# Performance work log

Measured on AMD Instinct MI355X. Metric: run time of the kernel, lower is better.

Reference implementation:

```python
import jax, jax.numpy as jnp
import numpy as np

EPS = 1e-10


def _entropy(feat):
    # feat: [B,S,D] -> [B,S]
    fa = jnp.abs(feat)
    fn = fa / (fa.sum(axis=-1, keepdims=True) + EPS)
    return -jnp.sum(fn * jnp.log(fn + EPS), axis=-1)


def setup_inputs() -> dict:
    key = jax.random.key(0)
    ks = jax.random.split(key, 16)
    B, S, H, C = 16, 1024, 512, 7
    inp = {
        'text': jax.random.normal(ks[0], (B, S, H), dtype=jnp.float32),
        'audio': jax.random.normal(ks[1], (B, S, H), dtype=jnp.float32),
        'visual': jax.random.normal(ks[2], (B, S, H), dtype=jnp.float32),
        'speaker_graph': jax.random.uniform(ks[3], (B, S, S), dtype=jnp.float32),
        'temporal_graph': jax.random.uniform(ks[4], (B, S, S), dtype=jnp.float32),
        'qmask': jax.random.randint(ks[5], (B, S), 0, 9, dtype=jnp.int64),
        # entropy gate linear: in = 3H+1, out = H  (stored as [in,out])
        'gate_W': jax.random.normal(ks[6], (3 * H + 1, H), dtype=jnp.float32) * 0.02,
        'gate_b': jnp.zeros((H,), dtype=jnp.float32),
        # spectral conv layers
        'W0': jax.random.normal(ks[7], (3 * H, H), dtype=jnp.float32) * 0.02,
        'b0': jnp.zeros((H,), dtype=jnp.float32),
        'W1': jax.random.normal(ks[8], (H, H), dtype=jnp.float32) * 0.02,
        'b1': jnp.zeros((H,), dtype=jnp.float32),
        'W2': jax.random.normal(ks[9], (H, H), dtype=jnp.float32) * 0.02,
        'b2': jnp.zeros((H,), dtype=jnp.float32),
        # classifier
        'Wc': jax.random.normal(ks[10], (H, C), dtype=jnp.float32) * 0.02,
        'bc': jnp.zeros((C,), dtype=jnp.float32),
    }
    return inp


def reference(text, audio, visual, speaker_graph, temporal_graph, qmask,
              gate_W, gate_b, W0, b0, W1, b1, W2, b2, Wc, bc):
    feats = {'text': text, 'audio': audio, 'visual': visual}
    names = list(feats.keys())

    # per-node entropy on speaker graph path (entropy_t computed but unused, as in source)
    ent_s = {m: _entropy(f) for m, f in feats.items()}

    # entropy-weighted gating per modality
    fused = {}
    for m in names:
        feat = feats[m]
        ref = jnp.mean(jnp.stack([feats[o] for o in names if o != m], axis=-1), axis=-1)
        gi = jnp.concatenate([feat, feat, ref, ent_s[m][..., None]], axis=-1)  # [B,S,3H+1]
        gate = jax.nn.sigmoid(gi @ gate_W + gate_b)
        fused[m] = gate * feat

    # spectral GNN: symmetric-normalized fused adjacency with self loops
    B, S = text.shape[0], text.shape[1]
    fused_adj = 0.5 * speaker_graph + 0.5 * temporal_graph
    fused_adj = fused_adj + jnp.eye(S, dtype=fused_adj.dtype)[None]
    D = fused_adj.sum(axis=-1)                                   # [B,S]
    dsi = jax.lax.rsqrt(D + EPS)                                  # (D+eps)^-0.5
    norm_adj = dsi[:, :, None] * fused_adj * dsi[:, None, :]      # [B,S,S]

    h = jnp.concatenate([fused['text'], fused['audio'], fused['visual']], axis=-1)  # [B,S,3H]
    for W, b in ((W0, b0), (W1, b1), (W2, b2)):
        h = jax.nn.relu(jnp.einsum('bij,bjd->bid', norm_adj, h @ W) + b)

    return h @ Wc + bc
```

## Files before the change

### kernel.cpp

```cpp
#include <hip/hip_runtime.h>
#include <hip/hip_bf16.h>
#include <hip/hip_fp16.h>

typedef _Float16 f16;
typedef __attribute__((ext_vector_type(8))) _Float16 f16x8;
typedef __attribute__((ext_vector_type(4))) _Float16 f16x4;
typedef __attribute__((ext_vector_type(4))) float f32x4;

#define BQ 16
#define SQ 1024
#define HQ 512
#define MQ (BQ*SQ)
#define PLANE ((size_t)MQ*512)

#define OFF_WG1T 0ul
#define OFF_WG2T 524288ul
#define OFF_W0T  1048576ul
#define OFF_W1T  2621440ul
#define OFF_W2T  3145728ul
#define OFF_WENT 3670016ul
#define OFF_ENTS 3672064ul
#define OFF_DSI  3868672ul
#define OFF_XF16 3934208ul
#define OFF_ANORM OFF_XF16
#define OFF_HN   (OFF_XF16 + 33554432ul)
#define OFF_T    71043072ul
#define OFF_YT   OFF_T
#define OFF_HCAT 104597504ul

__global__ __launch_bounds__(256) void k_prep(
    const float* __restrict__ gW, const float* __restrict__ W0,
    const float* __restrict__ W1, const float* __restrict__ W2,
    f16* __restrict__ Wg1t, f16* __restrict__ Wg2t, f16* __restrict__ W0t,
    f16* __restrict__ W1t, f16* __restrict__ W2t, float* __restrict__ went)
{
    int i = blockIdx.x * 256 + threadIdx.x;
    if (i < 1536*512) {
        int n = i & 511, k = i >> 9;
        W0t[(size_t)n*1536 + k] = (f16)W0[(size_t)k*512 + n];
    }
    if (i < 512*512) {
        int n = i >> 9, k = i & 511;
        float wa = gW[(size_t)k*512 + n];
        float wb = gW[(size_t)(512 + k)*512 + n];
        float wr = gW[(size_t)(1024 + k)*512 + n];
        Wg1t[(size_t)n*512 + k] = (f16)(wa + wb - 0.5f*wr);
        Wg2t[(size_t)n*512 + k] = (f16)(0.5f*wr);
        W1t[(size_t)n*512 + k]  = (f16)W1[(size_t)k*512 + n];
        W2t[(size_t)n*512 + k]  = (f16)W2[(size_t)k*512 + n];
    }
    if (i < 512) went[i] = gW[(size_t)1536*512 + i];
}

__global__ __launch_bounds__(256) void k_ent(
    const float* __restrict__ t, const float* __restrict__ a, const float* __restrict__ v,
    f16* __restrict__ xf, float* __restrict__ ents)
{
    int wave = threadIdx.x >> 6, lane = threadIdx.x & 63;
    int row = blockIdx.x * 4 + wave;
    const float* ptrs[3] = {t, a, v};
    float sum8[8];
#pragma unroll
    for (int j = 0; j < 8; j++) sum8[j] = 0.f;
#pragma unroll
    for (int m = 0; m < 3; m++) {
        const float4* p = (const float4*)(ptrs[m] + (size_t)row*512);
        float4 x0 = p[lane*2], x1 = p[lane*2 + 1];
        float xs[8] = {x0.x,x0.y,x0.z,x0.w,x1.x,x1.y,x1.z,x1.w};
        float s = 0.f;
#pragma unroll
        for (int j = 0; j < 8; j++) s += fabsf(xs[j]);
#pragma unroll
        for (int off = 32; off; off >>= 1) s += __shfl_xor(s, off);
        float inv = 1.f / (s + 1e-10f);
        float e = 0.f;
#pragma unroll
        for (int j = 0; j < 8; j++) { float fn = fabsf(xs[j])*inv; e += fn*__logf(fn + 1e-10f); }
#pragma unroll
        for (int off = 32; off; off >>= 1) e += __shfl_xor(e, off);
        if (lane == 0) ents[m*MQ + row] = -e;
        f16x8 o;
#pragma unroll
        for (int j = 0; j < 8; j++) o[j] = (f16)xs[j];
        *(f16x8*)(xf + ((size_t)m*MQ + row)*512 + lane*8) = o;
#pragma unroll
        for (int j = 0; j < 8; j++) sum8[j] += xs[j];
    }
    f16x8 o;
#pragma unroll
    for (int j = 0; j < 8; j++) o[j] = (f16)sum8[j];
    *(f16x8*)(xf + ((size_t)3*MQ + row)*512 + lane*8) = o;
}

__global__ __launch_bounds__(256) void k_dsi(
    const float* __restrict__ sp, const float* __restrict__ tg, float* __restrict__ dsi)
{
    int wave = threadIdx.x >> 6, lane = threadIdx.x & 63;
    int row = blockIdx.x * 4 + wave;
    const float4* p1 = (const float4*)(sp + (size_t)row*1024);
    const float4* p2 = (const float4*)(tg + (size_t)row*1024);
    float s = 0.f;
#pragma unroll
    for (int c = 0; c < 4; c++) {
        float4 x = p1[c*64 + lane], y = p2[c*64 + lane];
        s += x.x + x.y + x.z + x.w + y.x + y.y + y.z + y.w;
    }
#pragma unroll
    for (int off = 32; off; off >>= 1) s += __shfl_xor(s, off);
    if (lane == 0) dsi[row] = 1.f / sqrtf(0.5f*s + 1.f + 1e-10f);
}

__global__ __launch_bounds__(256) void k_anorm(
    const float* __restrict__ sp, const float* __restrict__ tg,
    const float* __restrict__ dsi, f16* __restrict__ an)
{
    size_t t = (size_t)blockIdx.x*256 + threadIdx.x;
    int j4 = (int)(t & 255) * 4;
    int i  = (int)(t >> 8) & 1023;
    int b  = (int)(t >> 18);
    size_t base = ((size_t)b << 20) + (size_t)i*1024 + j4;
    float4 x = *(const float4*)(sp + base);
    float4 y = *(const float4*)(tg + base);
    float4 dj = *(const float4*)(dsi + b*1024 + j4);
    float di = dsi[b*1024 + i];
    float v0 = 0.5f*(x.x + y.x) + (i == j4+0 ? 1.f : 0.f);
    float v1 = 0.5f*(x.y + y.y) + (i == j4+1 ? 1.f : 0.f);
    float v2 = 0.5f*(x.z + y.z) + (i == j4+2 ? 1.f : 0.f);
    float v3 = 0.5f*(x.w + y.w) + (i == j4+3 ? 1.f : 0.f);
    f16x4 o;
    o[0] = (f16)(di*v0*dj.x); o[1] = (f16)(di*v1*dj.y);
    o[2] = (f16)(di*v2*dj.z); o[3] = (f16)(di*v3*dj.w);
    *(f16x4*)(an + base) = o;
}

template<int MODE>
__global__ __launch_bounds__(256) void k_gemm(
    const f16* __restrict__ A, const f16* __restrict__ Bt, int K,
    float* __restrict__ fOut,
    const float* __restrict__ Tbuf, const float* __restrict__ entS,
    const float* __restrict__ went, const float* __restrict__ gb,
    const float* __restrict__ featf, f16* __restrict__ hOut, int hColOff,
    const float* __restrict__ bias)
{
    __shared__ f16 As[128][40];
    __shared__ f16 Bs[128][40];
    int tid = threadIdx.x;
    int lane = tid & 63, wave = tid >> 6;
    int wr = wave >> 1, wc = wave & 1;
    int m0 = blockIdx.x * 128, n0 = blockIdx.y * 128;
    int z = blockIdx.z;
    if constexpr (MODE == 3) {
        A  += (size_t)z * (1024*1024);
        Bt += (size_t)z * (512*1024);
    }
    int sr = tid >> 1, sc = (tid & 1) * 16;
    const f16* Ap = A  + (size_t)(m0 + sr)*K + sc;
    const f16* Bp = Bt + (size_t)(n0 + sr)*K + sc;
    f32x4 acc[4][4];
#pragma unroll
    for (int mi = 0; mi < 4; mi++)
#pragma unroll
        for (int ni = 0; ni < 4; ni++) acc[mi][ni] = (f32x4){0.f,0.f,0.f,0.f};
    int g = lane >> 4, r = lane & 15;
    for (int kt = 0; kt < K; kt += 32) {
        f16x8 av0 = *(const f16x8*)(Ap + kt);
        f16x8 av1 = *(const f16x8*)(Ap + kt + 8);
        f16x8 bv0 = *(const f16x8*)(Bp + kt);
        f16x8 bv1 = *(const f16x8*)(Bp + kt + 8);
        __syncthreads();
        *(f16x8*)&As[sr][sc]     = av0;
        *(f16x8*)&As[sr][sc + 8] = av1;
        *(f16x8*)&Bs[sr][sc]     = bv0;
        *(f16x8*)&Bs[sr][sc + 8] = bv1;
        __syncthreads();
        f16x8 af[4], bf[4];
#pragma unroll
        for (int mi = 0; mi < 4; mi++) af[mi] = *(const f16x8*)&As[wr*64 + mi*16 + r][g*8];
#pragma unroll
        for (int ni = 0; ni < 4; ni++) bf[ni] = *(const f16x8*)&Bs[wc*64 + ni*16 + r][g*8];
#pragma unroll
        for (int mi = 0; mi < 4; mi++)
#pragma unroll
            for (int ni = 0; ni < 4; ni++)
                acc[mi][ni] = __builtin_amdgcn_mfma_f32_16x16x32_f16(af[mi], bf[ni], acc[mi][ni], 0, 0, 0);
    }
#pragma unroll
    for (int mi = 0; mi < 4; mi++) {
        int row0 = m0 + wr*64 + mi*16 + g*4;
#pragma unroll
        for (int ni = 0; ni < 4; ni++) {
            int col = n0 + wc*64 + ni*16 + r;
            f32x4 v = acc[mi][ni];
            if constexpr (MODE == 0) {
#pragma unroll
                for (int j = 0; j < 4; j++)
                    fOut[(size_t)(row0 + j)*512 + col] = v[j];
            } else if constexpr (MODE == 1) {
                float wcol = went[col], gbc = gb[col];
#pragma unroll
                for (int j = 0; j < 4; j++) {
                    int row = row0 + j;
                    float val = v[j] + Tbuf[(size_t)row*512 + col] + entS[row]*wcol + gbc;
                    float gate = 1.f / (1.f + __expf(-val));
                    float o = gate * featf[(size_t)row*512 + col];
                    hOut[(size_t)row*1536 + hColOff + col] = (f16)o;
                }
            } else if constexpr (MODE == 2) {
                int bb = row0 >> 10, ml = row0 & 1023;
                f16x4 h4;
#pragma unroll
                for (int j = 0; j < 4; j++) h4[j] = (f16)v[j];
                *(f16x4*)(hOut + (((size_t)(bb*512 + col)) << 10) + ml) = h4;
            } else {
                float bcol = bias[col];
#pragma unroll
                for (int j = 0; j < 4; j++) {
                    float o = v[j] + bcol;
                    o = o > 0.f ? o : 0.f;
                    hOut[(size_t)(z*1024 + row0 + j)*512 + col] = (f16)o;
                }
            }
        }
    }
}

__global__ __launch_bounds__(256) void k_cls(
    const f16* __restrict__ h, const float* __restrict__ Wc,
    const float* __restrict__ bc, float* __restrict__ out)
{
    int wave = threadIdx.x >> 6, lane = threadIdx.x & 63;
    int row = blockIdx.x * 4 + wave;
    f16x8 hv = *(const f16x8*)(h + (size_t)row*512 + lane*8);
    float acc[7];
#pragma unroll
    for (int c = 0; c < 7; c++) acc[c] = 0.f;
#pragma unroll
    for (int j = 0; j < 8; j++) {
        float x = (float)hv[j];
        const float* wrow = Wc + (size_t)(lane*8 + j)*7;
#pragma unroll
        for (int c = 0; c < 7; c++) acc[c] += x * wrow[c];
    }
#pragma unroll
    for (int off = 32; off; off >>= 1)
#pragma unroll
        for (int c = 0; c < 7; c++) acc[c] += __shfl_xor(acc[c], off);
    if (lane == 0) {
#pragma unroll
        for (int c = 0; c < 7; c++) out[(size_t)row*7 + c] = acc[c] + bc[c];
    }
}

extern "C" void kernel_launch(void* const* d_in, const int* in_sizes, int n_in,
                              void* d_out, int out_size, void* d_ws, size_t ws_size,
                              hipStream_t stream) {
    (void)in_sizes; (void)n_in; (void)out_size; (void)ws_size;
    const float* text   = (const float*)d_in[0];
    const float* audio  = (const float*)d_in[1];
    const float* visual = (const float*)d_in[2];
    const float* spg    = (const float*)d_in[3];
    const float* tmg    = (const float*)d_in[4];
    const float* gW     = (const float*)d_in[6];
    const float* gb     = (const float*)d_in[7];
    const float* W0     = (const float*)d_in[8];
    const float* b0     = (const float*)d_in[9];
    const float* W1     = (const float*)d_in[10];
    const float* b1     = (const float*)d_in[11];
    const float* W2     = (const float*)d_in[12];
    const float* b2     = (const float*)d_in[13];
    const float* Wc     = (const float*)d_in[14];
    const float* bc     = (const float*)d_in[15];

    char* ws = (char*)d_ws;
    f16*   Wg1t = (f16*)(ws + OFF_WG1T);
    f16*   Wg2t = (f16*)(ws + OFF_WG2T);
    f16*   W0t  = (f16*)(ws + OFF_W0T);
    f16*   W1t  = (f16*)(ws + OFF_W1T);
    f16*   W2t  = (f16*)(ws + OFF_W2T);
    float* went = (float*)(ws + OFF_WENT);
    float* ents = (float*)(ws + OFF_ENTS);
    float* dsi  = (float*)(ws + OFF_DSI);
    f16*   xf   = (f16*)(ws + OFF_XF16);
    f16*   an   = (f16*)(ws + OFF_ANORM);
    f16*   hn   = (f16*)(ws + OFF_HN);
    float* Tbuf = (float*)(ws + OFF_T);
    f16*   yt   = (f16*)(ws + OFF_YT);
    f16*   hcat = (f16*)(ws + OFF_HCAT);
    float* outp = (float*)d_out;

    dim3 blk(256);
    k_prep<<<3072, blk, 0, stream>>>(gW, W0, W1, W2, Wg1t, Wg2t, W0t, W1t, W2t, went);
    k_ent<<<4096, blk, 0, stream>>>(text, audio, visual, xf, ents);
    k_dsi<<<4096, blk, 0, stream>>>(spg, tmg, dsi);

    k_gemm<0><<<dim3(128,4), blk, 0, stream>>>(xf + 3*PLANE, Wg2t, 512,
        Tbuf, nullptr, nullptr, nullptr, nullptr, nullptr, nullptr, 0, nullptr);
    k_gemm<1><<<dim3(128,4), blk, 0, stream>>>(xf + 0*PLANE, Wg1t, 512,
        nullptr, Tbuf, ents + 0*MQ, went, gb, text,   hcat, 0,    nullptr);
    k_gemm<1><<<dim3(128,4), blk, 0, stream>>>(xf + 1*PLANE, Wg1t, 512,
        nullptr, Tbuf, ents + 1*MQ, went, gb, audio,  hcat, 512,  nullptr);
    k_gemm<1><<<dim3(128,4), blk, 0, stream>>>(xf + 2*PLANE, Wg1t, 512,
        nullptr, Tbuf, ents + 2*MQ, went, gb, visual, hcat, 1024, nullptr);

    k_anorm<<<16384, blk, 0, stream>>>(spg, tmg, dsi, an);

    k_gemm<2><<<dim3(128,4), blk, 0, stream>>>(hcat, W0t, 1536,
        nullptr, nullptr, nullptr, nullptr, nullptr, nullptr, yt, 0, nullptr);
    k_gemm<3><<<dim3(8,4,16), blk, 0, stream>>>(an, yt, 1024,
        nullptr, nullptr, nullptr, nullptr, nullptr, nullptr, hn, 0, b0);
    k_gemm<2><<<dim3(128,4), blk, 0, stream>>>(hn, W1t, 512,
        nullptr, nullptr, nullptr, nullptr, nullptr, nullptr, yt, 0, nullptr);
    k_gemm<3><<<dim3(8,4,16), blk, 0, stream>>>(an, yt, 1024,
        nullptr, nullptr, nullptr, nullptr, nullptr, nullptr, hn, 0, b1);
    k_gemm<2><<<dim3(128,4), blk, 0, stream>>>(hn, W2t, 512,
        nullptr, nullptr, nullptr, nullptr, nullptr, nullptr, yt, 0, nullptr);
    k_gemm<3><<<dim3(8,4,16), blk, 0, stream>>>(an, yt, 1024,
        nullptr, nullptr, nullptr, nullptr, nullptr, nullptr, hn, 0, b2);

    k_cls<<<4096, blk, 0, stream>>>(hn, Wc, bc, outp);
}
```

Baseline: 642.1 us.

## Use direct global-to-LDS loads with XOR swizzle and K=64 tiles in GEMM

Reworks the shared GEMM main loop to load tiles with global_load_lds (direct global-to-LDS DMA) into an XOR-swizzled 128x64 layout, doubling the K step per barrier pair and avoiding register staging and bank conflicts. It also stores the gate's T buffer in fp16 instead of fp32 and reads the fp16 copies of the modality features in the gating epilogue instead of the fp32 originals, cutting epilogue memory traffic. The loop still uses single buffering with two barriers per tile, and the fp16 intermediates add rounding.

Result: faster. 551.8 us (-14.1%).

```diff
diff --git a/kernel.cpp b/kernel.cpp
--- a/kernel.cpp
+++ b/kernel.cpp
@@ -6,6 +6,8 @@
 typedef __attribute__((ext_vector_type(8))) _Float16 f16x8;
 typedef __attribute__((ext_vector_type(4))) _Float16 f16x4;
 typedef __attribute__((ext_vector_type(4))) float f32x4;
+typedef __attribute__((address_space(1))) const unsigned int gu32;
+typedef __attribute__((address_space(3))) unsigned int lu32;
 
 #define BQ 16
 #define SQ 1024
@@ -27,6 +29,12 @@
 #define OFF_T    71043072ul
 #define OFF_YT   OFF_T
 #define OFF_HCAT 104597504ul
+
+__device__ __forceinline__ void gl16(f16* lds, const f16* g) {
+    __builtin_amdgcn_global_load_lds(
+        (gu32*)(const __attribute__((address_space(1))) f16*)g,
+        (lu32*)(__attribute__((address_space(3))) f16*)lds, 16, 0, 0);
+}
 
 __global__ __launch_bounds__(256) void k_prep(
     const float* __restrict__ gW, const float* __restrict__ W0,
@@ -136,14 +144,13 @@
 template<int MODE>
 __global__ __launch_bounds__(256) void k_gemm(
     const f16* __restrict__ A, const f16* __restrict__ Bt, int K,
-    float* __restrict__ fOut,
-    const float* __restrict__ Tbuf, const float* __restrict__ entS,
+    const f16* __restrict__ Tbuf, const float* __restrict__ entS,
     const float* __restrict__ went, const float* __restrict__ gb,
-    const float* __restrict__ featf, f16* __restrict__ hOut, int hColOff,
+    const f16* __restrict__ featf, f16* __restrict__ hOut, int hColOff,
     const float* __restrict__ bias)
 {
-    __shared__ f16 As[128][40];
-    __shared__ f16 Bs[128][40];
+    __shared__ f16 As[128*64];
+    __shared__ f16 Bs[128*64];
     int tid = threadIdx.x;
     int lane = tid & 63, wave = tid >> 6;
     int wr = wave >> 1, wc = wave & 1;
@@ -153,36 +160,49 @@
         A  += (size_t)z * (1024*1024);
         Bt += (size_t)z * (512*1024);
     }
-    int sr = tid >> 1, sc = (tid & 1) * 16;
-    const f16* Ap = A  + (size_t)(m0 + sr)*K + sc;
-    const f16* Bp = Bt + (size_t)(n0 + sr)*K + sc;
+    int lrow = lane >> 3;
+    int swz  = (lane & 7) ^ lrow;
+    const f16* pA = A  + (size_t)(m0 + wave*32 + lrow)*K + swz*8;
+    const f16* pB = Bt + (size_t)(n0 + wave*32 + lrow)*K + swz*8;
+    f16* lA = As + (wave*4)*512;
+    f16* lB = Bs + (wave*4)*512;
+
     f32x4 acc[4][4];
 #pragma unroll
     for (int mi = 0; mi < 4; mi++)
 #pragma unroll
         for (int ni = 0; ni < 4; ni++) acc[mi][ni] = (f32x4){0.f,0.f,0.f,0.f};
     int g = lane >> 4, r = lane & 15;
-    for (int kt = 0; kt < K; kt += 32) {
-        f16x8 av0 = *(const f16x8*)(Ap + kt);
-        f16x8 av1 = *(const f16x8*)(Ap + kt + 8);
-        f16x8 bv0 = *(const f16x8*)(Bp + kt);
-        f16x8 bv1 = *(const f16x8*)(Bp + kt + 8);
+
+    for (int kt = 0; kt < K; kt += 64) {
         __syncthreads();
-        *(f16x8*)&As[sr][sc]     = av0;
-        *(f16x8*)&As[sr][sc + 8] = av1;
-        *(f16x8*)&Bs[sr][sc]     = bv0;
-        *(f16x8*)&Bs[sr][sc + 8] = bv1;
+#pragma unroll
+        for (int j = 0; j < 4; j++) {
+            gl16(lA + j*512, pA + (size_t)(j*8)*K + kt);
+            gl16(lB + j*512, pB + (size_t)(j*8)*K + kt);
+        }
         __syncthreads();
-        f16x8 af[4], bf[4];
-#pragma unroll
-        for (int mi = 0; mi < 4; mi++) af[mi] = *(const f16x8*)&As[wr*64 + mi*16 + r][g*8];
-#pragma unroll
-        for (int ni = 0; ni < 4; ni++) bf[ni] = *(const f16x8*)&Bs[wc*64 + ni*16 + r][g*8];
-#pragma unroll
-        for (int mi = 0; mi < 4; mi++)
-#pragma unroll
-            for (int ni = 0; ni < 4; ni++)
-                acc[mi][ni] = __builtin_amdgcn_mfma_f32_16x16x32_f16(af[mi], bf[ni], acc[mi][ni], 0, 0, 0);
+#pragma unroll
+        for (int kk = 0; kk < 2; kk++) {
+            f16x8 af[4], bf[4];
+#pragma unroll
+            for (int mi = 0; mi < 4; mi++) {
+                int row = wr*64 + mi*16 + r;
+                int ch = (kk*4 + g) ^ (row & 7);
+                af[mi] = *(const f16x8*)&As[row*64 + ch*8];
+            }
+#pragma unroll
+            for (int ni = 0; ni < 4; ni++) {
+                int row = wc*64 + ni*16 + r;
+                int ch = (kk*4 + g) ^ (row & 7);
+                bf[ni] = *(const f16x8*)&Bs[row*64 + ch*8];
+            }
+#pragma unroll
+            for (int mi = 0; mi < 4; mi++)
+#pragma unroll
+                for (int ni = 0; ni < 4; ni++)
+                    acc[mi][ni] = __builtin_amdgcn_mfma_f32_16x16x32_f16(af[mi], bf[ni], acc[mi][ni], 0, 0, 0);
+        }
     }
 #pragma unroll
     for (int mi = 0; mi < 4; mi++) {
@@ -194,15 +214,15 @@
             if constexpr (MODE == 0) {
 #pragma unroll
                 for (int j = 0; j < 4; j++)
-                    fOut[(size_t)(row0 + j)*512 + col] = v[j];
+                    hOut[(size_t)(row0 + j)*512 + col] = (f16)v[j];
             } else if constexpr (MODE == 1) {
                 float wcol = went[col], gbc = gb[col];
 #pragma unroll
                 for (int j = 0; j < 4; j++) {
                     int row = row0 + j;
-                    float val = v[j] + Tbuf[(size_t)row*512 + col] + entS[row]*wcol + gbc;
+                    float val = v[j] + (float)Tbuf[(size_t)row*512 + col] + entS[row]*wcol + gbc;
                     float gate = 1.f / (1.f + __expf(-val));
-                    float o = gate * featf[(size_t)row*512 + col];
+                    float o = gate * (float)featf[(size_t)row*512 + col];
                     hOut[(size_t)row*1536 + hColOff + col] = (f16)o;
                 }
             } else if constexpr (MODE == 2) {
@@ -283,7 +303,7 @@
     f16*   xf   = (f16*)(ws + OFF_XF16);
     f16*   an   = (f16*)(ws + OFF_ANORM);
     f16*   hn   = (f16*)(ws + OFF_HN);
-    float* Tbuf = (float*)(ws + OFF_T);
+    f16*   Tbuf = (f16*)(ws + OFF_T);
     f16*   yt   = (f16*)(ws + OFF_YT);
     f16*   hcat = (f16*)(ws + OFF_HCAT);
     float* outp = (float*)d_out;
@@ -294,28 +314,28 @@
     k_dsi<<<4096, blk, 0, stream>>>(spg, tmg, dsi);
 
     k_gemm<0><<<dim3(128,4), blk, 0, stream>>>(xf + 3*PLANE, Wg2t, 512,
-        Tbuf, nullptr, nullptr, nullptr, nullptr, nullptr, nullptr, 0, nullptr);
+        nullptr, nullptr, nullptr, nullptr, nullptr, Tbuf, 0, nullptr);
     k_gemm<1><<<dim3(128,4), blk, 0, stream>>>(xf + 0*PLANE, Wg1t, 512,
-        nullptr, Tbuf, ents + 0*MQ, went, gb, text,   hcat, 0,    nullptr);
+        Tbuf, ents + 0*MQ, went, gb, xf + 0*PLANE, hcat, 0,    nullptr);
     k_gemm<1><<<dim3(128,4), blk, 0, stream>>>(xf + 1*PLANE, Wg1t, 512,
-        nullptr, Tbuf, ents + 1*MQ, went, gb, audio,  hcat, 512,  nullptr);
+        Tbuf, ents + 1*MQ, went, gb, xf + 1*PLANE, hcat, 512,  nullptr);
     k_gemm<1><<<dim3(128,4), blk, 0, stream>>>(xf + 2*PLANE, Wg1t, 512,
-        nullptr, Tbuf, ents + 2*MQ, went, gb, visual, hcat, 1024, nullptr);
+        Tbuf, ents + 2*MQ, went, gb, xf + 2*PLANE, hcat, 1024, nullptr);
 
     k_anorm<<<16384, blk, 0, stream>>>(spg, tmg, dsi, an);
 
     k_gemm<2><<<dim3(128,4), blk, 0, stream>>>(hcat, W0t, 1536,
-        nullptr, nullptr, nullptr, nullptr, nullptr, nullptr, yt, 0, nullptr);
+        nullptr, nullptr, nullptr, nullptr, nullptr, yt, 0, nullptr);
     k_gemm<3><<<dim3(8,4,16), blk, 0, stream>>>(an, yt, 1024,
-        nullptr, nullptr, nullptr, nullptr, nullptr, nullptr, hn, 0, b0);
+        nullptr, nullptr, nullptr, nullptr, nullptr, hn, 0, b0);
     k_gemm<2><<<dim3(128,4), blk, 0, stream>>>(hn, W1t, 512,
-        nullptr, nullptr, nullptr, nullptr, nullptr, nullptr, yt, 0, nullptr);
+        nullptr, nullptr, nullptr, nullptr, nullptr, yt, 0, nullptr);
     k_gemm<3><<<dim3(8,4,16), blk, 0, stream>>>(an, yt, 1024,
-        nullptr, nullptr, nullptr, nullptr, nullptr, nullptr, hn, 0, b1);
+        nullptr, nullptr, nullptr, nullptr, nullptr, hn, 0, b1);
     k_gemm<2><<<dim3(128,4), blk, 0, stream>>>(hn, W2t, 512,
-        nullptr, nullptr, nullptr, nullptr, nullptr, nullptr, yt, 0, nullptr);
+        nullptr, nullptr, nullptr, nullptr, nullptr, yt, 0, nullptr);
     k_gemm<3><<<dim3(8,4,16), blk, 0, stream>>>(an, yt, 1024,
-        nullptr, nullptr, nullptr, nullptr, nullptr, nullptr, hn, 0, b2);
+        nullptr, nullptr, nullptr, nullptr, nullptr, hn, 0, b2);
 
     k_cls<<<4096, blk, 0, stream>>>(hn, Wc, bc, outp);
 }
```
